# Kernel tuning notes

Hardware: AMD Instinct MI355X
Metric: run time of the kernel (lower is better)

Reference implementation:

```python
import jax, jax.numpy as jnp
import numpy as np

NUM_HEADS = 4
KEY_DIM = 8
WINDOW = 4
SHIFT = 2
CHANNELS = 32


def setup_inputs() -> dict:
    key = jax.random.key(0)
    ks = jax.random.split(key, 9)
    C, H, D = CHANNELS, NUM_HEADS, KEY_DIM
    s = 0.05
    return {
        "x": jax.random.normal(ks[0], (4, 512, 512, C), jnp.float32),
        "Wq": jax.random.normal(ks[1], (C, H, D), jnp.float32) * s,
        "bq": jax.random.normal(ks[2], (H, D), jnp.float32) * s,
        "Wk": jax.random.normal(ks[3], (C, H, D), jnp.float32) * s,
        "bk": jax.random.normal(ks[4], (H, D), jnp.float32) * s,
        "Wv": jax.random.normal(ks[5], (C, H, D), jnp.float32) * s,
        "bv": jax.random.normal(ks[6], (H, D), jnp.float32) * s,
        "Wo": jax.random.normal(ks[7], (H, D, C), jnp.float32) * s,
        "bo": jax.random.normal(ks[8], (C,), jnp.float32) * s,
    }


def reference(x, Wq, bq, Wk, bk, Wv, bv, Wo, bo):
    B, H, W, C = x.shape
    ws, sh = WINDOW, SHIFT
    pad_h = (ws - H % ws) % ws
    pad_w = (ws - W % ws) % ws
    p = jnp.pad(x, ((0, 0), (0, pad_h), (0, pad_w), (0, 0)))
    if sh:
        p = jnp.roll(p, shift=(-sh, -sh), axis=(1, 2))
    Hp, Wp = H + pad_h, W + pad_w
    hw, ww = Hp // ws, Wp // ws
    # partition into windows: [B*hw*ww, ws*ws, C]
    win = p.reshape(B, hw, ws, ww, ws, C).transpose(0, 1, 3, 2, 4, 5)
    win = win.reshape(-1, ws * ws, C)
    # multi-head self-attention within each window (Keras MultiHeadAttention math)
    q = jnp.einsum('bnc,chd->bnhd', win, Wq) + bq
    k = jnp.einsum('bnc,chd->bnhd', win, Wk) + bk
    v = jnp.einsum('bnc,chd->bnhd', win, Wv) + bv
    scores = jnp.einsum('bqhd,bkhd->bhqk', q, k) / np.sqrt(KEY_DIM).astype(np.float32)
    attn = jax.nn.softmax(scores, axis=-1)
    o = jnp.einsum('bhqk,bkhd->bqhd', attn, v)
    out = jnp.einsum('bqhd,hdc->bqc', o, Wo) + bo
    # merge windows back: [B, Hp, Wp, C]
    out = out.reshape(B, hw, ww, ws, ws, C).transpose(0, 1, 3, 2, 4, 5)
    out = out.reshape(B, Hp, Wp, C)
    if sh:
        out = jnp.roll(out, shift=(sh, sh), axis=(1, 2))
    out = out[:, :H, :W, :]
    return x + out
```

## Files before the change

### kernel.cpp

```cpp
#include <hip/hip_runtime.h>
#include <hip/hip_bf16.h>
#include <stdint.h>

typedef float f32x4 __attribute__((ext_vector_type(4)));
typedef short s16x8 __attribute__((ext_vector_type(8)));
typedef unsigned short u16;
typedef u16 u16x4 __attribute__((ext_vector_type(4)));

__device__ __align__(16) float g_tbl[16 * 256];

__device__ __forceinline__ u16 f2bf(float f) {
    union { __hip_bfloat16 h; u16 u; } cv;
    cv.h = __float2bfloat16(f);
    return cv.u;
}
__device__ __forceinline__ int pkbf(float lo, float hi) {
    return (int)(unsigned)f2bf(lo) | ((int)(unsigned)f2bf(hi) << 16);
}
__device__ __forceinline__ f32x4 mfma16(s16x8 a, s16x8 b, f32x4 c) {
    return __builtin_amdgcn_mfma_f32_16x16x32_bf16(a, b, c, 0, 0, 0);
}
__device__ __forceinline__ float exp2_hw(float x) {
    float r; asm("v_exp_f32 %0, %1" : "=v"(r) : "v"(x)); return r;
}
__device__ __forceinline__ int swz16(int v) {
    return __builtin_amdgcn_ds_swizzle(v, 0x401F);
}
__device__ __forceinline__ int xor32i(int v, bool lo32) {
    auto r = __builtin_amdgcn_permlane32_swap(v, v, false, false);
    return lo32 ? r[1] : r[0];
}
__device__ __forceinline__ int pl_lo_to_hi(int v) {
    auto r = __builtin_amdgcn_permlane32_swap(v, v, false, false);
    return r[0];
}
__device__ __forceinline__ s16x8 frag4(int d0, int d1, int d2, int d3) {
    union { int i[4]; s16x8 v; } u;
    u.i[0] = d0; u.i[1] = d1; u.i[2] = d2; u.i[3] = d3;
    return u.v;
}
#define C_FENCE() asm volatile("" ::: "memory")

__global__ void setup_kernel(
    const float* __restrict__ Wq, const float* __restrict__ bq,
    const float* __restrict__ Wk, const float* __restrict__ bk,
    const float* __restrict__ Wv, const float* __restrict__ bv,
    const float* __restrict__ Wo, const float* __restrict__ bo)
{
    const int lane = threadIdx.x & 63;
    if (threadIdx.x >= 64) return;
    const int c16 = lane & 15;
    const int g   = lane >> 4;
    const float qscale = 0.35355339059327373f * 1.4426950408889634f;

    f32x4* T = (f32x4*)g_tbl;
    union { s16x8 s; f32x4 f; } cv;

    #pragma unroll
    for (int j = 0; j < 6; ++j) {
        const float* Wsrc = (j < 2) ? Wq : (j < 4) ? Wk : Wv;
        const int colW = ((j & 1) << 4) | c16;
        const float sc = (j < 2) ? qscale : 1.0f;
        s16x8 wf;
        #pragma unroll
        for (int jj = 0; jj < 8; ++jj)
            wf[jj] = (short)f2bf(Wsrc[(g * 8 + jj) * 32 + colW] * sc);
        cv.s = wf;
        T[j * 64 + lane] = cv.f;
    }
    #pragma unroll
    for (int j2 = 0; j2 < 2; ++j2) {
        const int cout = j2 * 16 + c16;
        s16x8 wf;
        #pragma unroll
        for (int jj = 0; jj < 8; ++jj) {
            const int h = (g >> 1) * 2 + (jj >> 2);
            const int d = 4 * (g & 1) + (jj & 3);
            wf[jj] = (short)f2bf(Wo[(h * 8 + d) * 32 + cout]);
        }
        cv.s = wf;
        T[(6 + j2) * 64 + lane] = cv.f;
    }
    #pragma unroll
    for (int j = 0; j < 4; ++j) {
        const float* bsrc = (j < 2) ? bq : bk;
        const float sc = (j < 2) ? qscale : 1.0f;
        f32x4 b;
        #pragma unroll
        for (int i = 0; i < 4; ++i)
            b[i] = bsrc[((j & 1) << 4) + 4 * g + i] * sc;
        T[(8 + j) * 64 + lane] = b;
    }
    #pragma unroll
    for (int jv = 0; jv < 2; ++jv) {
        float b = bv[jv * 16 + c16];
        T[(12 + jv) * 64 + lane] = (f32x4){b, b, b, b};
    }
    #pragma unroll
    for (int j2 = 0; j2 < 2; ++j2) {
        f32x4 b;
        #pragma unroll
        for (int i = 0; i < 4; ++i)
            b[i] = bo[j2 * 16 + 4 * g + i];
        T[(14 + j2) * 64 + lane] = b;
    }
}

__global__ __launch_bounds__(256) void swin_attn_kernel(
    const float* __restrict__ x, float* __restrict__ out)
{
    const int lane  = threadIdx.x & 63;
    const int wave  = threadIdx.x >> 6;
    const int c16   = lane & 15;
    const int g     = lane >> 4;
    const bool lo32 = (lane < 32);

    __shared__ __align__(16) u16 qk[4][16][88];
    __shared__ __align__(16) u16 vT[4][33][24];
    __shared__ __align__(16) u16 pB[4][17][24];

    {
        const int col = (g < 2) ? (32 + 4 * g) : (72 + 4 * (g - 2));
        *(u16x4*)&qk[wave][c16][col] = (u16x4){0, 0, 0, 0};
        if (lane < 6) *(u16x4*)&vT[wave][32][lane * 4] = (u16x4){0, 0, 0, 0};
        if (lane < 6) *(u16x4*)&pB[wave][16][lane * 4] = (u16x4){0, 0, 0, 0};
    }
    C_FENCE();

    const f32x4* T = (const f32x4*)g_tbl;
    f32x4 u[16];
    #pragma unroll
    for (int k = 0; k < 16; ++k) u[k] = T[k * 64 + lane];
    union { f32x4 f; s16x8 s; } cv;
    s16x8 wqkv[6], wo_frag[2];
    #pragma unroll
    for (int j = 0; j < 6; ++j) { cv.f = u[j]; wqkv[j] = cv.s; }
    cv.f = u[6]; wo_frag[0] = cv.s;
    cv.f = u[7]; wo_frag[1] = cv.s;
    f32x4 bias_qk[4] = {u[8], u[9], u[10], u[11]};
    f32x4 bias_v[2]  = {u[12], u[13]};
    f32x4 bo_frag[2] = {u[14], u[15]};

    const f32x4 zero4 = {0.f, 0.f, 0.f, 0.f};

    const u16* ap_base = (g == 0) ? &qk[wave][c16][40] : &qk[wave][c16][72];
    const u16* bp_base = (g == 0) ? &qk[wave][c16][0]  : &qk[wave][c16][32];
    const int  hstep   = (g == 0) ? 8 : 0;
    const u16* pp      = (g < 2) ? &pB[wave][c16][g * 8] : &pB[wave][16][0];
    const u16* vp_base = (g < 2) ? &vT[wave][c16 & 7][g * 8] : &vT[wave][32][0];
    const int  vstep   = (g < 2) ? 8 * 24 : 0;

    const int wbase = (blockIdx.x * 4 + wave) * 4;
    long curpix;
    f32x4 px0, px1;
    {
        const int w = wbase;
        const int b = w >> 14, rem = w & 16383, wi = rem >> 7, wj = rem & 127;
        const int row  = (wi * 4 + (c16 >> 2) + 2) & 511;
        const int colp = (wj * 4 + (c16 & 3) + 2) & 511;
        curpix = ((((long)b << 9) + row) * 512 + colp) * 32;
        px0 = *(const f32x4*)(x + curpix + g * 8);
        px1 = *(const f32x4*)(x + curpix + g * 8 + 4);
    }

    #pragma unroll 1
    for (int it = 0; it < 4; ++it) {
        const long pixbase = curpix;
        s16x8 xfrag = frag4(pkbf(px0[0], px0[1]), pkbf(px0[2], px0[3]),
                            pkbf(px1[0], px1[1]), pkbf(px1[2], px1[3]));

        #pragma unroll
        for (int j = 0; j < 4; ++j) {
            f32x4 c = mfma16(wqkv[j], xfrag, bias_qk[j]);
            const int col = (j < 2) ? (j * 16 + 4 * g) : (40 + (j - 2) * 16 + 4 * g);
            u16x4 qv;
            #pragma unroll
            for (int i = 0; i < 4; ++i) qv[i] = f2bf(c[i]);
            *(u16x4*)&qk[wave][c16][col] = qv;
        }
        #pragma unroll
        for (int jv = 0; jv < 2; ++jv) {
            f32x4 c = mfma16(xfrag, wqkv[4 + jv], bias_v[jv]);
            u16x4 vv;
            #pragma unroll
            for (int i = 0; i < 4; ++i) vv[i] = f2bf(c[i]);
            *(u16x4*)&vT[wave][jv * 16 + c16][4 * g] = vv;
        }

        {
            const int w = wbase + ((it + 1) & 3);
            const int b = w >> 14, rem = w & 16383, wi = rem >> 7, wj = rem & 127;
            const int row  = (wi * 4 + (c16 >> 2) + 2) & 511;
            const int colp = (wj * 4 + (c16 & 3) + 2) & 511;
            const long np = ((((long)b << 9) + row) * 512 + colp) * 32;
            px0 = *(const f32x4*)(x + np + g * 8);
            px1 = *(const f32x4*)(x + np + g * 8 + 4);
            curpix = np;
        }
        f32x4 r0 = *(const f32x4*)(x + pixbase + 4 * g);
        f32x4 r1 = *(const f32x4*)(x + pixbase + 16 + 4 * g);

        C_FENCE();

        f32x4 o_acc[4];
        #pragma unroll
        for (int h = 0; h < 4; ++h) {
            s16x8 afrag = *(const s16x8*)(ap_base + h * hstep);
            s16x8 bfrag = *(const s16x8*)(bp_base + h * hstep);
            f32x4 s = mfma16(afrag, bfrag, zero4);

            float e0 = exp2_hw(s[0]), e1 = exp2_hw(s[1]);
            float e2 = exp2_hw(s[2]), e3 = exp2_hw(s[3]);
            float part = (e0 + e1) + (e2 + e3);
            float sum  = part + __int_as_float(swz16(__float_as_int(part)));
            sum += __int_as_float(xor32i(__float_as_int(sum), lo32));
            const float inv = __builtin_amdgcn_rcpf(sum);
            u16x4 pv;
            pv[0] = f2bf(e0 * inv); pv[1] = f2bf(e1 * inv);
            pv[2] = f2bf(e2 * inv); pv[3] = f2bf(e3 * inv);
            *(u16x4*)&pB[wave][c16][4 * g] = pv;
            C_FENCE();

            s16x8 vfrag = *(const s16x8*)(vp_base + h * vstep);
            s16x8 pfrag = *(const s16x8*)pp;
            o_acc[h] = mfma16(vfrag, pfrag, zero4);
            C_FENCE();
        }

        int t00 = pkbf(o_acc[0][0], o_acc[0][1]), t01 = pkbf(o_acc[0][2], o_acc[0][3]);
        int t10 = pkbf(o_acc[1][0], o_acc[1][1]), t11 = pkbf(o_acc[1][2], o_acc[1][3]);
        int t20 = pkbf(o_acc[2][0], o_acc[2][1]), t21 = pkbf(o_acc[2][2], o_acc[2][3]);
        int t30 = pkbf(o_acc[3][0], o_acc[3][1]), t31 = pkbf(o_acc[3][2], o_acc[3][3]);
        int m20 = pl_lo_to_hi(t20), m21 = pl_lo_to_hi(t21);
        int m30 = pl_lo_to_hi(t30), m31 = pl_lo_to_hi(t31);
        s16x8 ofrag = frag4(lo32 ? t00 : m20, lo32 ? t01 : m21,
                            lo32 ? t10 : m30, lo32 ? t11 : m31);

        f32x4 ci0 = bo_frag[0], ci1 = bo_frag[1];
        #pragma unroll
        for (int i = 0; i < 4; ++i) { ci0[i] += r0[i]; ci1[i] += r1[i]; }
        f32x4 c0 = mfma16(wo_frag[0], ofrag, ci0);
        f32x4 c1 = mfma16(wo_frag[1], ofrag, ci1);
        *(f32x4*)(out + pixbase + 4 * g) = c0;
        *(f32x4*)(out + pixbase + 16 + 4 * g) = c1;

        C_FENCE();
    }
}

extern "C" void kernel_launch(void* const* d_in, const int* in_sizes, int n_in,
                              void* d_out, int out_size, void* d_ws, size_t ws_size,
                              hipStream_t stream) {
    const float* x  = (const float*)d_in[0];
    const float* Wq = (const float*)d_in[1];
    const float* bq = (const float*)d_in[2];
    const float* Wk = (const float*)d_in[3];
    const float* bk = (const float*)d_in[4];
    const float* Wv = (const float*)d_in[5];
    const float* bv = (const float*)d_in[6];
    const float* Wo = (const float*)d_in[7];
    const float* bo = (const float*)d_in[8];
    float* out = (float*)d_out;

    hipLaunchKernelGGL(setup_kernel, dim3(1), dim3(64), 0, stream,
                       Wq, bq, Wk, bk, Wv, bv, Wo, bo);
    hipLaunchKernelGGL(swin_attn_kernel, dim3(4096), dim3(256), 0, stream,
                       x, out);
}
```

Measured before the change: 65.27 us.

## Interleave two windows per iteration with double shared buffers for ILP

Each wave now processes two attention windows at once, with two copies of the Q/K, V and P shared-memory scratch, and interleaves their MFMA, exp and softmax chains. This hides the latency of the serial MFMA-to-LDS-to-MFMA dependency chain within a single wave and halves the loop trip count. The cost is twice the LDS footprint and more live registers, which may lower occupancy.

```diff
diff --git a/kernel.cpp b/kernel.cpp
--- a/kernel.cpp
+++ b/kernel.cpp
@@ -55,7 +55,6 @@
 
     f32x4* T = (f32x4*)g_tbl;
     union { s16x8 s; f32x4 f; } cv;
-
     #pragma unroll
     for (int j = 0; j < 6; ++j) {
         const float* Wsrc = (j < 2) ? Wq : (j < 4) ? Wk : Wv;
@@ -115,15 +114,16 @@
     const int g     = lane >> 4;
     const bool lo32 = (lane < 32);
 
-    __shared__ __align__(16) u16 qk[4][16][88];
-    __shared__ __align__(16) u16 vT[4][33][24];
-    __shared__ __align__(16) u16 pB[4][17][24];
-
-    {
+    __shared__ __align__(16) u16 qk[2][4][16][88];
+    __shared__ __align__(16) u16 vT[2][4][33][24];
+    __shared__ __align__(16) u16 pB[2][4][17][24];
+
+    #pragma unroll
+    for (int par = 0; par < 2; ++par) {
         const int col = (g < 2) ? (32 + 4 * g) : (72 + 4 * (g - 2));
-        *(u16x4*)&qk[wave][c16][col] = (u16x4){0, 0, 0, 0};
-        if (lane < 6) *(u16x4*)&vT[wave][32][lane * 4] = (u16x4){0, 0, 0, 0};
-        if (lane < 6) *(u16x4*)&pB[wave][16][lane * 4] = (u16x4){0, 0, 0, 0};
+        *(u16x4*)&qk[par][wave][c16][col] = (u16x4){0, 0, 0, 0};
+        if (lane < 6) *(u16x4*)&vT[par][wave][32][lane * 4] = (u16x4){0, 0, 0, 0};
+        if (lane < 6) *(u16x4*)&pB[par][wave][16][lane * 4] = (u16x4){0, 0, 0, 0};
     }
     C_FENCE();
 
@@ -143,106 +143,151 @@
 
     const f32x4 zero4 = {0.f, 0.f, 0.f, 0.f};
 
-    const u16* ap_base = (g == 0) ? &qk[wave][c16][40] : &qk[wave][c16][72];
-    const u16* bp_base = (g == 0) ? &qk[wave][c16][0]  : &qk[wave][c16][32];
-    const int  hstep   = (g == 0) ? 8 : 0;
-    const u16* pp      = (g < 2) ? &pB[wave][c16][g * 8] : &pB[wave][16][0];
-    const u16* vp_base = (g < 2) ? &vT[wave][c16 & 7][g * 8] : &vT[wave][32][0];
-    const int  vstep   = (g < 2) ? 8 * 24 : 0;
+    const int hstep = (g == 0) ? 8 : 0;
+    const int vstep = (g < 2) ? 8 * 24 : 0;
+    const u16 *ap[2], *bp[2], *pp[2], *vp[2];
+    #pragma unroll
+    for (int par = 0; par < 2; ++par) {
+        ap[par] = (g == 0) ? &qk[par][wave][c16][40] : &qk[par][wave][c16][72];
+        bp[par] = (g == 0) ? &qk[par][wave][c16][0]  : &qk[par][wave][c16][32];
+        pp[par] = (g < 2) ? &pB[par][wave][c16][g * 8] : &pB[par][wave][16][0];
+        vp[par] = (g < 2) ? &vT[par][wave][c16 & 7][g * 8] : &vT[par][wave][32][0];
+    }
 
     const int wbase = (blockIdx.x * 4 + wave) * 4;
-    long curpix;
-    f32x4 px0, px1;
-    {
-        const int w = wbase;
+    auto pixaddr = [&](int w) -> long {
         const int b = w >> 14, rem = w & 16383, wi = rem >> 7, wj = rem & 127;
         const int row  = (wi * 4 + (c16 >> 2) + 2) & 511;
         const int colp = (wj * 4 + (c16 & 3) + 2) & 511;
-        curpix = ((((long)b << 9) + row) * 512 + colp) * 32;
-        px0 = *(const f32x4*)(x + curpix + g * 8);
-        px1 = *(const f32x4*)(x + curpix + g * 8 + 4);
-    }
+        return ((((long)b << 9) + row) * 512 + colp) * 32;
+    };
+
+    long pixA = pixaddr(wbase), pixB = pixaddr(wbase + 1);
+    f32x4 pxA0 = *(const f32x4*)(x + pixA + g * 8);
+    f32x4 pxA1 = *(const f32x4*)(x + pixA + g * 8 + 4);
+    f32x4 pxB0 = *(const f32x4*)(x + pixB + g * 8);
+    f32x4 pxB1 = *(const f32x4*)(x + pixB + g * 8 + 4);
 
     #pragma unroll 1
-    for (int it = 0; it < 4; ++it) {
-        const long pixbase = curpix;
-        s16x8 xfrag = frag4(pkbf(px0[0], px0[1]), pkbf(px0[2], px0[3]),
-                            pkbf(px1[0], px1[1]), pkbf(px1[2], px1[3]));
+    for (int kk = 0; kk < 2; ++kk) {
+        const long pbA = pixA, pbB = pixB;
+        s16x8 xfA = frag4(pkbf(pxA0[0], pxA0[1]), pkbf(pxA0[2], pxA0[3]),
+                          pkbf(pxA1[0], pxA1[1]), pkbf(pxA1[2], pxA1[3]));
+        s16x8 xfB = frag4(pkbf(pxB0[0], pxB0[1]), pkbf(pxB0[2], pxB0[3]),
+                          pkbf(pxB1[0], pxB1[1]), pkbf(pxB1[2], pxB1[3]));
 
         #pragma unroll
         for (int j = 0; j < 4; ++j) {
-            f32x4 c = mfma16(wqkv[j], xfrag, bias_qk[j]);
+            f32x4 cA = mfma16(wqkv[j], xfA, bias_qk[j]);
+            f32x4 cB = mfma16(wqkv[j], xfB, bias_qk[j]);
             const int col = (j < 2) ? (j * 16 + 4 * g) : (40 + (j - 2) * 16 + 4 * g);
-            u16x4 qv;
+            u16x4 qa, qb;
             #pragma unroll
-            for (int i = 0; i < 4; ++i) qv[i] = f2bf(c[i]);
-            *(u16x4*)&qk[wave][c16][col] = qv;
+            for (int i = 0; i < 4; ++i) { qa[i] = f2bf(cA[i]); qb[i] = f2bf(cB[i]); }
+            *(u16x4*)&qk[0][wave][c16][col] = qa;
+            *(u16x4*)&qk[1][wave][c16][col] = qb;
         }
         #pragma unroll
         for (int jv = 0; jv < 2; ++jv) {
-            f32x4 c = mfma16(xfrag, wqkv[4 + jv], bias_v[jv]);
-            u16x4 vv;
+            f32x4 cA = mfma16(xfA, wqkv[4 + jv], bias_v[jv]);
+            f32x4 cB = mfma16(xfB, wqkv[4 + jv], bias_v[jv]);
+            u16x4 va, vb;
             #pragma unroll
-            for (int i = 0; i < 4; ++i) vv[i] = f2bf(c[i]);
-            *(u16x4*)&vT[wave][jv * 16 + c16][4 * g] = vv;
+            for (int i = 0; i < 4; ++i) { va[i] = f2bf(cA[i]); vb[i] = f2bf(cB[i]); }
+            *(u16x4*)&vT[0][wave][jv * 16 + c16][4 * g] = va;
+            *(u16x4*)&vT[1][wave][jv * 16 + c16][4 * g] = vb;
         }
 
         {
-            const int w = wbase + ((it + 1) & 3);
-            const int b = w >> 14, rem = w & 16383, wi = rem >> 7, wj = rem & 127;
-            const int row  = (wi * 4 + (c16 >> 2) + 2) & 511;
-            const int colp = (wj * 4 + (c16 & 3) + 2) & 511;
-            const long np = ((((long)b << 9) + row) * 512 + colp) * 32;
-            px0 = *(const f32x4*)(x + np + g * 8);
-            px1 = *(const f32x4*)(x + np + g * 8 + 4);
-            curpix = np;
-        }
-        f32x4 r0 = *(const f32x4*)(x + pixbase + 4 * g);
-        f32x4 r1 = *(const f32x4*)(x + pixbase + 16 + 4 * g);
+            const int nA = wbase + ((2 * kk + 2) & 3);
+            const int nB = wbase + ((2 * kk + 3) & 3);
+            pixA = pixaddr(nA); pixB = pixaddr(nB);
+            pxA0 = *(const f32x4*)(x + pixA + g * 8);
+            pxA1 = *(const f32x4*)(x + pixA + g * 8 + 4);
+            pxB0 = *(const f32x4*)(x + pixB + g * 8);
+            pxB1 = *(const f32x4*)(x + pixB + g * 8 + 4);
+        }
+        f32x4 rA0 = *(const f32x4*)(x + pbA + 4 * g);
+        f32x4 rA1 = *(const f32x4*)(x + pbA + 16 + 4 * g);
+        f32x4 rB0 = *(const f32x4*)(x + pbB + 4 * g);
+        f32x4 rB1 = *(const f32x4*)(x + pbB + 16 + 4 * g);
 
         C_FENCE();
 
-        f32x4 o_acc[4];
+        f32x4 oA[4], oB[4];
         #pragma unroll
         for (int h = 0; h < 4; ++h) {
-            s16x8 afrag = *(const s16x8*)(ap_base + h * hstep);
-            s16x8 bfrag = *(const s16x8*)(bp_base + h * hstep);
-            f32x4 s = mfma16(afrag, bfrag, zero4);
-
-            float e0 = exp2_hw(s[0]), e1 = exp2_hw(s[1]);
-            float e2 = exp2_hw(s[2]), e3 = exp2_hw(s[3]);
-            float part = (e0 + e1) + (e2 + e3);
-            float sum  = part + __int_as_float(swz16(__float_as_int(part)));
-            sum += __int_as_float(xor32i(__float_as_int(sum), lo32));
-            const float inv = __builtin_amdgcn_rcpf(sum);
-            u16x4 pv;
-            pv[0] = f2bf(e0 * inv); pv[1] = f2bf(e1 * inv);
-            pv[2] = f2bf(e2 * inv); pv[3] = f2bf(e3 * inv);
-            *(u16x4*)&pB[wave][c16][4 * g] = pv;
+            s16x8 afA = *(const s16x8*)(ap[0] + h * hstep);
+            s16x8 bfA = *(const s16x8*)(bp[0] + h * hstep);
+            s16x8 afB = *(const s16x8*)(ap[1] + h * hstep);
+            s16x8 bfB = *(const s16x8*)(bp[1] + h * hstep);
+            f32x4 sA = mfma16(afA, bfA, zero4);
+            f32x4 sB = mfma16(afB, bfB, zero4);
+
+            float a0 = exp2_hw(sA[0]), a1 = exp2_hw(sA[1]);
+            float a2 = exp2_hw(sA[2]), a3 = exp2_hw(sA[3]);
+            float b0 = exp2_hw(sB[0]), b1 = exp2_hw(sB[1]);
+            float b2 = exp2_hw(sB[2]), b3 = exp2_hw(sB[3]);
+            float partA = (a0 + a1) + (a2 + a3);
+            float partB = (b0 + b1) + (b2 + b3);
+            float sumA = partA + __int_as_float(swz16(__float_as_int(partA)));
+            float sumB = partB + __int_as_float(swz16(__float_as_int(partB)));
+            sumA += __int_as_float(xor32i(__float_as_int(sumA), lo32));
+            sumB += __int_as_float(xor32i(__float_as_int(sumB), lo32));
+            const float invA = __builtin_amdgcn_rcpf(sumA);
+            const float invB = __builtin_amdgcn_rcpf(sumB);
+            u16x4 pa, pb;
+            pa[0] = f2bf(a0 * invA); pa[1] = f2bf(a1 * invA);
+            pa[2] = f2bf(a2 * invA); pa[3] = f2bf(a3 * invA);
+            pb[0] = f2bf(b0 * invB); pb[1] = f2bf(b1 * invB);
+            pb[2] = f2bf(b2 * invB); pb[3] = f2bf(b3 * invB);
+            *(u16x4*)&pB[0][wave][c16][4 * g] = pa;
+            *(u16x4*)&pB[1][wave][c16][4 * g] = pb;
             C_FENCE();
 
-            s16x8 vfrag = *(const s16x8*)(vp_base + h * vstep);
-            s16x8 pfrag = *(const s16x8*)pp;
-            o_acc[h] = mfma16(vfrag, pfrag, zero4);
+            s16x8 vfA = *(const s16x8*)(vp[0] + h * vstep);
+            s16x8 pfA = *(const s16x8*)pp[0];
+            s16x8 vfB = *(const s16x8*)(vp[1] + h * vstep);
+            s16x8 pfB = *(const s16x8*)pp[1];
+            oA[h] = mfma16(vfA, pfA, zero4);
+            oB[h] = mfma16(vfB, pfB, zero4);
             C_FENCE();
         }
 
-        int t00 = pkbf(o_acc[0][0], o_acc[0][1]), t01 = pkbf(o_acc[0][2], o_acc[0][3]);
-        int t10 = pkbf(o_acc[1][0], o_acc[1][1]), t11 = pkbf(o_acc[1][2], o_acc[1][3]);
-        int t20 = pkbf(o_acc[2][0], o_acc[2][1]), t21 = pkbf(o_acc[2][2], o_acc[2][3]);
-        int t30 = pkbf(o_acc[3][0], o_acc[3][1]), t31 = pkbf(o_acc[3][2], o_acc[3][3]);
-        int m20 = pl_lo_to_hi(t20), m21 = pl_lo_to_hi(t21);
-        int m30 = pl_lo_to_hi(t30), m31 = pl_lo_to_hi(t31);
-        s16x8 ofrag = frag4(lo32 ? t00 : m20, lo32 ? t01 : m21,
-                            lo32 ? t10 : m30, lo32 ? t11 : m31);
-
-        f32x4 ci0 = bo_frag[0], ci1 = bo_frag[1];
-        #pragma unroll
-        for (int i = 0; i < 4; ++i) { ci0[i] += r0[i]; ci1[i] += r1[i]; }
-        f32x4 c0 = mfma16(wo_frag[0], ofrag, ci0);
-        f32x4 c1 = mfma16(wo_frag[1], ofrag, ci1);
-        *(f32x4*)(out + pixbase + 4 * g) = c0;
-        *(f32x4*)(out + pixbase + 16 + 4 * g) = c1;
+        {
+            int t00 = pkbf(oA[0][0], oA[0][1]), t01 = pkbf(oA[0][2], oA[0][3]);
+            int t10 = pkbf(oA[1][0], oA[1][1]), t11 = pkbf(oA[1][2], oA[1][3]);
+            int t20 = pkbf(oA[2][0], oA[2][1]), t21 = pkbf(oA[2][2], oA[2][3]);
+            int t30 = pkbf(oA[3][0], oA[3][1]), t31 = pkbf(oA[3][2], oA[3][3]);
+            int m20 = pl_lo_to_hi(t20), m21 = pl_lo_to_hi(t21);
+            int m30 = pl_lo_to_hi(t30), m31 = pl_lo_to_hi(t31);
+            s16x8 ofrag = frag4(lo32 ? t00 : m20, lo32 ? t01 : m21,
+                                lo32 ? t10 : m30, lo32 ? t11 : m31);
+            f32x4 ci0 = bo_frag[0], ci1 = bo_frag[1];
+            #pragma unroll
+            for (int i = 0; i < 4; ++i) { ci0[i] += rA0[i]; ci1[i] += rA1[i]; }
+            f32x4 c0 = mfma16(wo_frag[0], ofrag, ci0);
+            f32x4 c1 = mfma16(wo_frag[1], ofrag, ci1);
+            *(f32x4*)(out + pbA + 4 * g) = c0;
+            *(f32x4*)(out + pbA + 16 + 4 * g) = c1;
+        }
+        {
+            int t00 = pkbf(oB[0][0], oB[0][1]), t01 = pkbf(oB[0][2], oB[0][3]);
+            int t10 = pkbf(oB[1][0], oB[1][1]), t11 = pkbf(oB[1][2], oB[1][3]);
+            int t20 = pkbf(oB[2][0], oB[2][1]), t21 = pkbf(oB[2][2], oB[2][3]);
+            int t30 = pkbf(oB[3][0], oB[3][1]), t31 = pkbf(oB[3][2], oB[3][3]);
+            int m20 = pl_lo_to_hi(t20), m21 = pl_lo_to_hi(t21);
+            int m30 = pl_lo_to_hi(t30), m31 = pl_lo_to_hi(t31);
+            s16x8 ofrag = frag4(lo32 ? t00 : m20, lo32 ? t01 : m21,
+                                lo32 ? t10 : m30, lo32 ? t11 : m31);
+            f32x4 ci0 = bo_frag[0], ci1 = bo_frag[1];
+            #pragma unroll
+            for (int i = 0; i < 4; ++i) { ci0[i] += rB0[i]; ci1[i] += rB1[i]; }
+            f32x4 c0 = mfma16(wo_frag[0], ofrag, ci0);
+            f32x4 c1 = mfma16(wo_frag[1], ofrag, ci1);
+            *(f32x4*)(out + pbB + 4 * g) = c0;
+            *(f32x4*)(out + pbB + 16 + 4 * g) = c1;
+        }
 
         C_FENCE();
     }
```

Measured after the change: 73.64 us. 1.13x slower.
